# Kernel optimization log

Measured on AMD Instinct MI355X. Metric: run time of the kernel, lower is better.

## Reference

```python
import jax, jax.numpy as jnp
import numpy as np
import math

NO, NR, E = 100000, 1000, 1000000
DO, DR, DE, H, OM = 64, 32, 4, 64, 32


def setup_inputs() -> dict:
    key = jax.random.key(0)
    ks = jax.random.split(key, 20)
    s = lambda k, sh: jax.random.normal(k, sh, dtype=jnp.float32) * 0.05
    inp = {
        'x_order': jax.random.normal(ks[0], (NO, DO), dtype=jnp.float32),
        'x_rider': jax.random.normal(ks[1], (NR, DR), dtype=jnp.float32),
        'edge_attr': jax.random.normal(ks[2], (E, DE), dtype=jnp.float32),
        'order_idx': jax.random.randint(ks[3], (E,), 0, NO),
        'rider_idx': jax.random.randint(ks[4], (E,), 0, NR),
        'omega_encoded': jax.random.normal(ks[5], (OM,), dtype=jnp.float32),
        # TransformerConv params (heads=1)
        'Wk': s(ks[6], (DO, H)), 'bk': jnp.zeros((H,), jnp.float32),
        'Wq': s(ks[7], (DR, H)), 'bq': jnp.zeros((H,), jnp.float32),
        'Wv': s(ks[8], (DO, H)), 'bv': jnp.zeros((H,), jnp.float32),
        'We': s(ks[9], (DE, H)),  # lin_edge, bias=False in PyG
        'Wskip': s(ks[10], (DR, H)), 'bskip': jnp.zeros((H,), jnp.float32),
        # order_proj
        'Wp': s(ks[11], (DO, H)), 'bp': jnp.zeros((H,), jnp.float32),
        # residual MLP: Linear(2H+OM,128) -> ReLU -> Linear(128,1)
        'W1': s(ks[12], (2 * H + OM, 128)), 'b1': jnp.zeros((128,), jnp.float32),
        'W2': s(ks[13], (128, 1)), 'b2': jnp.zeros((1,), jnp.float32),
    }
    return inp


def _segment_softmax(alpha, seg, num_segments):
    m = jax.ops.segment_max(alpha, seg, num_segments=num_segments)
    m = jnp.where(jnp.isfinite(m), m, 0.0)
    ex = jnp.exp(alpha - m[seg])
    denom = jax.ops.segment_sum(ex, seg, num_segments=num_segments)
    return ex / (denom[seg] + 1e-16)


def reference(x_order, x_rider, edge_attr, order_idx, rider_idx, omega_encoded,
              Wk, bk, Wq, bq, Wv, bv, We, Wskip, bskip, Wp, bp, W1, b1, W2, b2):
    scale = 1.0 / math.sqrt(H)
    # TransformerConv((order, rider) -> rider), heads=1, edge_dim
    q = x_rider @ Wq + bq            # [NR, H]
    k = x_order @ Wk + bk            # [NO, H]
    v = x_order @ Wv + bv            # [NO, H]
    e = edge_attr @ We               # [E, H]
    k_j = k[order_idx] + e           # [E, H]
    v_j = v[order_idx] + e           # [E, H]
    alpha = jnp.sum(q[rider_idx] * k_j, axis=-1) * scale  # [E]
    alpha = _segment_softmax(alpha, rider_idx, NR)
    agg = jax.ops.segment_sum(alpha[:, None] * v_j, rider_idx, num_segments=NR)  # [NR, H]
    rider_emb = agg + x_rider @ Wskip + bskip  # root/skip connection

    # edge scoring
    order_proj = x_order @ Wp + bp   # [NO, H]
    oe = order_proj[order_idx]       # [E, H]
    re = rider_emb[rider_idx]        # [E, H]
    dot = jnp.sum(oe * re, axis=-1) * scale  # [E]
    omega_expand = jnp.broadcast_to(omega_encoded[None, :], (oe.shape[0], OM))
    resid_in = jnp.concatenate([oe, re, omega_expand], axis=-1)  # [E, 2H+OM]
    hmid = jax.nn.relu(resid_in @ W1 + b1)
    resid = (hmid @ W2 + b2)[:, 0]
    return jnp.clip(dot + resid, -10.0, 10.0)
```

## Files before the change

kernel.cpp:

```cpp
#include <hip/hip_runtime.h>
#include <hip/hip_bf16.h>
#include <math.h>

#define NO_N 100000
#define NR_N 1000
#define E_N  1000000
#define SB     250
#define SCHUNK 4000
#define KVP_TILES 1563
#define MAXTILES 17008

typedef short bf16x8 __attribute__((ext_vector_type(8)));
typedef float floatx4 __attribute__((ext_vector_type(4)));

__device__ __forceinline__ unsigned short bfu(float x) {
    union { __hip_bfloat16 h; unsigned short u; } c;
    c.h = __float2bfloat16(x);
    return c.u;
}
__device__ __forceinline__ float bflo(unsigned int u) {
    return __uint_as_float(u << 16);
}
__device__ __forceinline__ float bfhi(unsigned int u) {
    return __uint_as_float(u & 0xffff0000u);
}

__global__ __launch_bounds__(256) void k_prep_rider(
    const float* __restrict__ xr,
    const float* __restrict__ Wq, const float* __restrict__ bq,
    const float* __restrict__ Wskip, const float* __restrict__ bskip,
    const float* __restrict__ We,
    float* __restrict__ q, float* __restrict__ skip, float* __restrict__ t)
{
    __shared__ float sx[4][32];
    __shared__ float sq[4][64];
    int tid = threadIdx.x;
    int rbase = blockIdx.x * 4;
    if (tid < 128) {
        int rl = tid >> 5, d = tid & 31;
        int r = rbase + rl;
        sx[rl][d] = (r < NR_N) ? xr[r * 32 + d] : 0.f;
    }
    __syncthreads();
    int rl = tid >> 6, h = tid & 63;
    int r = rbase + rl;
    float aq = bq[h], as = bskip[h];
    #pragma unroll 4
    for (int d = 0; d < 32; ++d) {
        float xv = sx[rl][d];
        aq += xv * Wq[d * 64 + h];
        as += xv * Wskip[d * 64 + h];
    }
    sq[rl][h] = aq;
    if (r < NR_N) { q[r * 64 + h] = aq; skip[r * 64 + h] = as; }
    __syncthreads();
    if (tid < 16) {
        int rl2 = tid >> 2, d = tid & 3;
        int r2 = rbase + rl2;
        float acc = 0.f;
        for (int hh = 0; hh < 64; ++hh) acc += We[d * 64 + hh] * sq[rl2][hh];
        if (r2 < NR_N) t[r2 * 4 + d] = acc;
    }
}

__global__ __launch_bounds__(128) void k_prep_b1eff(
    const float* __restrict__ W1, const float* __restrict__ b1,
    const float* __restrict__ omega, float* __restrict__ b1eff)
{
    int c = threadIdx.x;
    float acc = b1[c];
    #pragma unroll 4
    for (int j = 0; j < 32; ++j) acc += omega[j] * W1[(128 + j) * 128 + c];
    b1eff[c] = acc;
}

__global__ __launch_bounds__(256) void k_kvp(
    const float* __restrict__ x,
    const float* __restrict__ Wk, const float* __restrict__ bk,
    const float* __restrict__ Wv, const float* __restrict__ bv,
    const float* __restrict__ Wp, const float* __restrict__ bp,
    unsigned short* __restrict__ kb, unsigned short* __restrict__ vb,
    unsigned short* __restrict__ pb)
{
    __shared__ __align__(16) unsigned short sX[64 * 72];
    const int tid = threadIdx.x;
    const int wave = tid >> 6, lane = tid & 63;
    const int l15 = lane & 15, quad = lane >> 4;

    bf16x8 bfr[3][2];
    float bias[3];
    unsigned short* outT[3];
    int colc[3];
    #pragma unroll
    for (int ct = 0; ct < 3; ++ct) {
        int n = wave * 48 + ct * 16 + l15;
        int table = n >> 6, c = n & 63;
        const float* W  = (table == 0) ? Wk : (table == 1) ? Wv : Wp;
        const float* bb = (table == 0) ? bk : (table == 1) ? bv : bp;
        bias[ct] = bb[c];
        colc[ct] = c;
        outT[ct] = (table == 0) ? kb : (table == 1) ? vb : pb;
        #pragma unroll
        for (int kf = 0; kf < 2; ++kf) {
            bf16x8 f;
            #pragma unroll
            for (int j = 0; j < 8; ++j)
                f[j] = (short)bfu(W[(size_t)(kf * 32 + quad * 8 + j) * 64 + c]);
            bfr[ct][kf] = f;
        }
    }

    const int srl = tid >> 2;
    const int sqt = (tid & 3) * 16;

    for (int tile = blockIdx.x; tile < KVP_TILES; tile += gridDim.x) {
        int rowbase = tile * 64;
        {
            int row = rowbase + srl;
            unsigned short* dst = sX + srl * 72 + sqt;
            if (row < NO_N) {
                const float4* src = (const float4*)(x + (size_t)row * 64 + sqt);
                #pragma unroll
                for (int i = 0; i < 4; ++i) {
                    float4 a = src[i];
                    ushort4 u = { bfu(a.x), bfu(a.y), bfu(a.z), bfu(a.w) };
                    *(ushort4*)(dst + i * 4) = u;
                }
            } else {
                ushort4 z = {0, 0, 0, 0};
                #pragma unroll
                for (int i = 0; i < 4; ++i) *(ushort4*)(dst + i * 4) = z;
            }
        }
        __syncthreads();

        floatx4 acc[4][3];
        #pragma unroll
        for (int rt = 0; rt < 4; ++rt)
            #pragma unroll
            for (int ct = 0; ct < 3; ++ct)
                acc[rt][ct] = (floatx4){bias[ct], bias[ct], bias[ct], bias[ct]};

        #pragma unroll
        for (int rt = 0; rt < 4; ++rt) {
            const unsigned short* ar = sX + (size_t)(rt * 16 + l15) * 72 + quad * 8;
            bf16x8 a0 = *(const bf16x8*)(ar);
            bf16x8 a1 = *(const bf16x8*)(ar + 32);
            #pragma unroll
            for (int ct = 0; ct < 3; ++ct) {
                floatx4 c = acc[rt][ct];
                c = __builtin_amdgcn_mfma_f32_16x16x32_bf16(a0, bfr[ct][0], c, 0, 0, 0);
                c = __builtin_amdgcn_mfma_f32_16x16x32_bf16(a1, bfr[ct][1], c, 0, 0, 0);
                acc[rt][ct] = c;
            }
        }

        #pragma unroll
        for (int rt = 0; rt < 4; ++rt) {
            int rb = rowbase + rt * 16 + quad * 4;
            #pragma unroll
            for (int ct = 0; ct < 3; ++ct) {
                unsigned short* o = outT[ct];
                size_t cbase = colc[ct];
                #pragma unroll
                for (int g = 0; g < 4; ++g) {
                    int row = rb + g;
                    if (row < NO_N)
                        o[(size_t)row * 64 + cbase] = bfu(acc[rt][ct][g]);
                }
            }
        }
        __syncthreads();
    }
}

__global__ __launch_bounds__(256) void k_hist2(const int* __restrict__ ridx,
                                               int* __restrict__ ghist)
{
    __shared__ int hc[NR_N];
    int tid = threadIdx.x, b = blockIdx.x;
    for (int i = tid; i < NR_N; i += 256) hc[i] = 0;
    __syncthreads();
    int s = b * SCHUNK;
    for (int i = s + tid; i < s + SCHUNK; i += 256)
        atomicAdd(&hc[ridx[i]], 1);
    __syncthreads();
    for (int i = tid; i < NR_N; i += 256)
        ghist[i * SB + b] = hc[i];
}

__global__ __launch_bounds__(256) void k_colscan(const int* __restrict__ ghist,
                                                 int* __restrict__ gpre,
                                                 int* __restrict__ counts)
{
    __shared__ int s[256];
    int tid = threadIdx.x, r = blockIdx.x;
    int v = (tid < SB) ? ghist[r * SB + tid] : 0;
    s[tid] = v;
    __syncthreads();
    for (int off = 1; off < 256; off <<= 1) {
        int tv = (tid >= off) ? s[tid - off] : 0;
        __syncthreads();
        s[tid] += tv;
        __syncthreads();
    }
    if (tid < SB) gpre[r * SB + tid] = s[tid] - v;
    if (tid == 255) counts[r] = s[255];
}

__global__ __launch_bounds__(1024) void k_scan(const int* __restrict__ counts,
                                               int* __restrict__ offsets,
                                               int* __restrict__ tilestart,
                                               int* __restrict__ tile2r)
{
    __shared__ int s[1024];
    int tid = threadIdx.x;
    int c = (tid < NR_N) ? counts[tid] : 0;
    s[tid] = c;
    __syncthreads();
    for (int off = 1; off < 1024; off <<= 1) {
        int tv = (tid >= off) ? s[tid - off] : 0;
        __syncthreads();
        s[tid] += tv;
        __syncthreads();
    }
    if (tid < NR_N) offsets[tid] = s[tid] - c;
    if (tid == NR_N - 1) offsets[NR_N] = s[tid];
    __syncthreads();
    int tc = (tid < NR_N) ? ((c + 63) >> 6) : 0;
    s[tid] = tc;
    __syncthreads();
    for (int off = 1; off < 1024; off <<= 1) {
        int tv = (tid >= off) ? s[tid - off] : 0;
        __syncthreads();
        s[tid] += tv;
        __syncthreads();
    }
    if (tid < NR_N) {
        int ts = s[tid] - tc;
        tilestart[tid] = ts;
        for (int t = 0; t < tc; ++t) tile2r[ts + t] = tid;
    }
    if (tid == NR_N - 1) tilestart[NR_N] = s[tid];
}

__global__ __launch_bounds__(256) void k_scatter2(
    const int* __restrict__ ridx, const int* __restrict__ oidx,
    const float* __restrict__ ea, const float* __restrict__ t,
    const int* __restrict__ offsets, const int* __restrict__ gpre,
    int4* __restrict__ spack, int2* __restrict__ soe)
{
    __shared__ int cur[NR_N];
    int tid = threadIdx.x, b = blockIdx.x;
    for (int i = tid; i < NR_N; i += 256)
        cur[i] = offsets[i] + gpre[i * SB + b];
    __syncthreads();
    int s = b * SCHUNK;
    for (int i = s + tid; i < s + SCHUNK; i += 256) {
        int r = ridx[i];
        int o = oidx[i];
        float4 e4 = *(const float4*)(ea + (size_t)i * 4);
        float4 t4 = *(const float4*)(t + r * 4);
        float h = e4.x * t4.x + e4.y * t4.y + e4.z * t4.z + e4.w * t4.w;
        int pos = atomicAdd(&cur[r], 1);
        int4 pk;
        pk.x = o;
        pk.y = __float_as_int(h);
        pk.z = (int)((unsigned)bfu(e4.x) | ((unsigned)bfu(e4.y) << 16));
        pk.w = (int)((unsigned)bfu(e4.z) | ((unsigned)bfu(e4.w) << 16));
        spack[pos] = pk;
        soe[pos] = make_int2(o, i);
    }
}

__global__ __launch_bounds__(1024) void k_rider(
    const int* __restrict__ offsets, const int4* __restrict__ spack,
    const float* __restrict__ q,
    const unsigned short* __restrict__ kb, const unsigned short* __restrict__ vb,
    const float* __restrict__ We, const float* __restrict__ skip,
    float* __restrict__ emb)
{
    __shared__ float sQ[64];
    __shared__ int2 sOX[16][64];
    __shared__ float rv[16][64];
    __shared__ float re4[16][4];
    __shared__ float rd[16];

    int r = blockIdx.x;
    int wave = threadIdx.x >> 6, lane = threadIdx.x & 63;
    if (threadIdx.x < 64) sQ[threadIdx.x] = q[r * 64 + threadIdx.x];
    __syncthreads();

    int beg = offsets[r], end = offsets[r + 1];
    int cnt = end - beg;
    int chunk = (cnt + 15) >> 4;
    int s0 = beg + wave * chunk;
    int s1 = min(s0 + chunk, end);

    float aggv = 0.f, dsum = 0.f;
    float ag0 = 0.f, ag1 = 0.f, ag2 = 0.f, ag3 = 0.f;
    const float2* sQ2 = (const float2*)sQ;

    for (int jb = s0; jb < s1; jb += 64) {
        int j = jb + lane;
        bool valid = (j < s1);
        int4 pk = make_int4(0, 0, 0, 0);
        if (valid) pk = spack[j];
        int oo = pk.x;
        float h = __int_as_float(pk.y);

        const uint4* krow = (const uint4*)(kb + (size_t)oo * 64);
        uint4 K0 = krow[0], K1 = krow[1], K2 = krow[2], K3 = krow[3];
        uint4 K4 = krow[4], K5 = krow[5], K6 = krow[6], K7 = krow[7];
        float acc = h;
        #define DOT8(Kv, base) { \
            float2 qa = sQ2[(base) + 0]; \
            acc = fmaf(bflo(Kv.x), qa.x, acc); acc = fmaf(bfhi(Kv.x), qa.y, acc); \
            float2 qb = sQ2[(base) + 1]; \
            acc = fmaf(bflo(Kv.y), qb.x, acc); acc = fmaf(bfhi(Kv.y), qb.y, acc); \
            float2 qc = sQ2[(base) + 2]; \
            acc = fmaf(bflo(Kv.z), qc.x, acc); acc = fmaf(bfhi(Kv.z), qc.y, acc); \
            float2 qd = sQ2[(base) + 3]; \
            acc = fmaf(bflo(Kv.w), qd.x, acc); acc = fmaf(bfhi(Kv.w), qd.y, acc); }
        DOT8(K0, 0) DOT8(K1, 4) DOT8(K2, 8) DOT8(K3, 12)
        DOT8(K4, 16) DOT8(K5, 20) DOT8(K6, 24) DOT8(K7, 28)
        #undef DOT8

        float exv = valid ? __expf(acc * 0.125f) : 0.f;
        dsum += exv;
        unsigned int ez = (unsigned int)pk.z, ew = (unsigned int)pk.w;
        ag0 = fmaf(exv, bflo(ez), ag0);
        ag1 = fmaf(exv, bfhi(ez), ag1);
        ag2 = fmaf(exv, bflo(ew), ag2);
        ag3 = fmaf(exv, bfhi(ew), ag3);

        sOX[wave][lane] = make_int2(oo, __float_as_int(exv));

        int nn = min(s1 - jb, 64);
        int i = 0;
        for (; i + 8 <= nn; i += 8) {
            int2 x0 = sOX[wave][i + 0], x1 = sOX[wave][i + 1];
            int2 x2 = sOX[wave][i + 2], x3 = sOX[wave][i + 3];
            int2 x4 = sOX[wave][i + 4], x5 = sOX[wave][i + 5];
            int2 x6 = sOX[wave][i + 6], x7 = sOX[wave][i + 7];
            unsigned short u0 = vb[(size_t)x0.x * 64 + lane];
            unsigned short u1 = vb[(size_t)x1.x * 64 + lane];
            unsigned short u2 = vb[(size_t)x2.x * 64 + lane];
            unsigned short u3 = vb[(size_t)x3.x * 64 + lane];
            unsigned short u4 = vb[(size_t)x4.x * 64 + lane];
            unsigned short u5 = vb[(size_t)x5.x * 64 + lane];
            unsigned short u6 = vb[(size_t)x6.x * 64 + lane];
            unsigned short u7 = vb[(size_t)x7.x * 64 + lane];
            aggv = fmaf(__int_as_float(x0.y), __uint_as_float((unsigned int)u0 << 16), aggv);
            aggv = fmaf(__int_as_float(x1.y), __uint_as_float((unsigned int)u1 << 16), aggv);
            aggv = fmaf(__int_as_float(x2.y), __uint_as_float((unsigned int)u2 << 16), aggv);
            aggv = fmaf(__int_as_float(x3.y), __uint_as_float((unsigned int)u3 << 16), aggv);
            aggv = fmaf(__int_as_float(x4.y), __uint_as_float((unsigned int)u4 << 16), aggv);
            aggv = fmaf(__int_as_float(x5.y), __uint_as_float((unsigned int)u5 << 16), aggv);
            aggv = fmaf(__int_as_float(x6.y), __uint_as_float((unsigned int)u6 << 16), aggv);
            aggv = fmaf(__int_as_float(x7.y), __uint_as_float((unsigned int)u7 << 16), aggv);
        }
        for (; i < nn; ++i) {
            int2 xx = sOX[wave][i];
            unsigned short uu = vb[(size_t)xx.x * 64 + lane];
            aggv = fmaf(__int_as_float(xx.y), __uint_as_float((unsigned int)uu << 16), aggv);
        }
    }

    #pragma unroll
    for (int m = 1; m < 64; m <<= 1) {
        dsum += __shfl_xor(dsum, m);
        ag0 += __shfl_xor(ag0, m);
        ag1 += __shfl_xor(ag1, m);
        ag2 += __shfl_xor(ag2, m);
        ag3 += __shfl_xor(ag3, m);
    }

    rv[wave][lane] = aggv;
    if (lane == 0) {
        rd[wave] = dsum;
        re4[wave][0] = ag0; re4[wave][1] = ag1;
        re4[wave][2] = ag2; re4[wave][3] = ag3;
    }
    __syncthreads();
    if (threadIdx.x < 64) {
        int l = threadIdx.x;
        float av = 0.f, ds = 0.f, a0 = 0.f, a1 = 0.f, a2 = 0.f, a3 = 0.f;
        #pragma unroll 4
        for (int w = 0; w < 16; ++w) {
            av += rv[w][l]; ds += rd[w];
            a0 += re4[w][0]; a1 += re4[w][1]; a2 += re4[w][2]; a3 += re4[w][3];
        }
        float corr = a0 * We[0 * 64 + l] + a1 * We[1 * 64 + l]
                   + a2 * We[2 * 64 + l] + a3 * We[3 * 64 + l];
        emb[r * 64 + l] = (av + corr) / (ds + 1e-16f) + skip[r * 64 + l];
    }
}

__global__ __launch_bounds__(256) void k_br(
    const float* __restrict__ emb, const float* __restrict__ W1,
    const float* __restrict__ b1eff, float* __restrict__ Br)
{
    int wave = threadIdx.x >> 6, lane = threadIdx.x & 63;
    int r = blockIdx.x * 4 + wave;
    if (r >= NR_N) return;
    float a0 = b1eff[lane], a1 = b1eff[64 + lane];
    #pragma unroll 8
    for (int d = 0; d < 64; ++d) {
        float ev = emb[r * 64 + d];
        a0 = fmaf(ev, W1[(size_t)(64 + d) * 128 + lane], a0);
        a1 = fmaf(ev, W1[(size_t)(64 + d) * 128 + 64 + lane], a1);
    }
    Br[r * 128 + lane] = a0;
    Br[r * 128 + 64 + lane] = a1;
}

__global__ __launch_bounds__(256) void k_edge2(
    const int2* __restrict__ soe, const int* __restrict__ offsets,
    const int* __restrict__ tilestart, const int* __restrict__ tile2r,
    const unsigned short* __restrict__ pb, const float* __restrict__ emb,
    const float* __restrict__ Br, const float* __restrict__ W1,
    const float* __restrict__ W2, const float* __restrict__ b2,
    float* __restrict__ out)
{
    __shared__ __align__(16) unsigned short sA[64 * 72];
    __shared__ float sDot[64];
    __shared__ int   sE[64];
    __shared__ float sPart[4][64];

    const int tid = threadIdx.x;
    const int wave = tid >> 6;
    const int lane = tid & 63;
    const int l15 = lane & 15;
    const int quad = lane >> 4;

    bf16x8 bfr[2][2];
    float w2v[2];
    #pragma unroll
    for (int ctl = 0; ctl < 2; ++ctl) {
        int n = wave * 32 + ctl * 16 + l15;
        w2v[ctl] = W2[n];
        #pragma unroll
        for (int kc = 0; kc < 2; ++kc) {
            bf16x8 f;
            #pragma unroll
            for (int j = 0; j < 8; ++j)
                f[j] = (short)bfu(W1[(size_t)(kc * 32 + quad * 8 + j) * 128 + n]);
            bfr[ctl][kc] = f;
        }
    }
    float b2v = b2[0];
    const int ntiles = tilestart[NR_N];

    const int el = tid >> 2;
    const int q16 = (tid & 3) * 16;

    for (int tile = blockIdx.x; tile < ntiles; tile += gridDim.x) {
        int r = tile2r[tile];
        int jb = offsets[r] + ((tile - tilestart[r]) << 6);
        int jend = offsets[r + 1];

        {
            int j = jb + el;
            int o = 0, e = -1;
            if (j < jend) { int2 oe = soe[j]; o = oe.x; e = oe.y; }
            const uint4* po = (const uint4*)(pb + (size_t)o * 64 + q16);
            uint4 A0 = po[0], A1 = po[1];
            const float4* pe = (const float4*)(emb + r * 64 + q16);
            float4 e0 = pe[0], e1 = pe[1], e2 = pe[2], e3 = pe[3];
            float dotp;
            dotp  = bflo(A0.x) * e0.x + bfhi(A0.x) * e0.y;
            dotp += bflo(A0.y) * e0.z + bfhi(A0.y) * e0.w;
            dotp += bflo(A0.z) * e1.x + bfhi(A0.z) * e1.y;
            dotp += bflo(A0.w) * e1.z + bfhi(A0.w) * e1.w;
            dotp += bflo(A1.x) * e2.x + bfhi(A1.x) * e2.y;
            dotp += bflo(A1.y) * e2.z + bfhi(A1.y) * e2.w;
            dotp += bflo(A1.z) * e3.x + bfhi(A1.z) * e3.y;
            dotp += bflo(A1.w) * e3.z + bfhi(A1.w) * e3.w;
            uint4* sp = (uint4*)(sA + el * 72 + q16);
            sp[0] = A0; sp[1] = A1;
            dotp += __shfl_xor(dotp, 1);
            dotp += __shfl_xor(dotp, 2);
            if ((tid & 3) == 0) { sDot[el] = dotp; sE[el] = e; }
        }
        __syncthreads();

        float brv[2];
        #pragma unroll
        for (int ctl = 0; ctl < 2; ++ctl)
            brv[ctl] = Br[r * 128 + wave * 32 + ctl * 16 + l15];

        floatx4 acc[4][2];
        #pragma unroll
        for (int rt = 0; rt < 4; ++rt)
            #pragma unroll
            for (int ctl = 0; ctl < 2; ++ctl)
                acc[rt][ctl] = (floatx4){0.f, 0.f, 0.f, 0.f};

        #pragma unroll
        for (int rt = 0; rt < 4; ++rt) {
            const unsigned short* ar = sA + (size_t)(rt * 16 + l15) * 72 + quad * 8;
            bf16x8 a0 = *(const bf16x8*)(ar);
            bf16x8 a1 = *(const bf16x8*)(ar + 32);
            #pragma unroll
            for (int ctl = 0; ctl < 2; ++ctl) {
                floatx4 c = acc[rt][ctl];
                c = __builtin_amdgcn_mfma_f32_16x16x32_bf16(a0, bfr[ctl][0], c, 0, 0, 0);
                c = __builtin_amdgcn_mfma_f32_16x16x32_bf16(a1, bfr[ctl][1], c, 0, 0, 0);
                acc[rt][ctl] = c;
            }
        }

        #pragma unroll
        for (int rt = 0; rt < 4; ++rt) {
            floatx4 s;
            #pragma unroll
            for (int g = 0; g < 4; ++g)
                s[g] = fmaxf(acc[rt][0][g] + brv[0], 0.f) * w2v[0]
                     + fmaxf(acc[rt][1][g] + brv[1], 0.f) * w2v[1];
            #pragma unroll
            for (int m = 1; m < 16; m <<= 1) {
                s[0] += __shfl_xor(s[0], m);
                s[1] += __shfl_xor(s[1], m);
                s[2] += __shfl_xor(s[2], m);
                s[3] += __shfl_xor(s[3], m);
            }
            if (l15 == 0) {
                int rowb = rt * 16 + quad * 4;
                sPart[wave][rowb + 0] = s[0];
                sPart[wave][rowb + 1] = s[1];
                sPart[wave][rowb + 2] = s[2];
                sPart[wave][rowb + 3] = s[3];
            }
        }
        __syncthreads();
        if (tid < 64) {
            int e = sE[tid];
            if (e >= 0) {
                float v = sPart[0][tid] + sPart[1][tid] + sPart[2][tid] + sPart[3][tid]
                        + 0.125f * sDot[tid] + b2v;
                out[e] = fminf(fmaxf(v, -10.f), 10.f);
            }
        }
        __syncthreads();
    }
}

extern "C" void kernel_launch(void* const* d_in, const int* in_sizes, int n_in,
                              void* d_out, int out_size, void* d_ws, size_t ws_size,
                              hipStream_t stream)
{
    const float* x_order   = (const float*)d_in[0];
    const float* x_rider   = (const float*)d_in[1];
    const float* edge_attr = (const float*)d_in[2];
    const int*   order_idx = (const int*)d_in[3];
    const int*   rider_idx = (const int*)d_in[4];
    const float* omega     = (const float*)d_in[5];
    const float* Wk = (const float*)d_in[6];  const float* bk = (const float*)d_in[7];
    const float* Wq = (const float*)d_in[8];  const float* bq = (const float*)d_in[9];
    const float* Wv = (const float*)d_in[10]; const float* bv = (const float*)d_in[11];
    const float* We = (const float*)d_in[12];
    const float* Wskip = (const float*)d_in[13]; const float* bskip = (const float*)d_in[14];
    const float* Wp = (const float*)d_in[15]; const float* bp = (const float*)d_in[16];
    const float* W1 = (const float*)d_in[17]; const float* b1 = (const float*)d_in[18];
    const float* W2 = (const float*)d_in[19]; const float* b2 = (const float*)d_in[20];
    float* out = (float*)d_out;

    unsigned short* ws_kb = (unsigned short*)d_ws;
    unsigned short* ws_vb = ws_kb + (size_t)NO_N * 64;
    unsigned short* ws_pb = ws_vb + (size_t)NO_N * 64;
    int4* ws_spack = (int4*)(ws_pb + (size_t)NO_N * 64);
    int2* ws_soe   = (int2*)(ws_spack + E_N);
    float* wsf     = (float*)(ws_soe + E_N);
    float* ws_q    = wsf;
    float* ws_skip = ws_q + NR_N * 64;
    float* ws_emb  = ws_skip + NR_N * 64;
    float* ws_t    = ws_emb + NR_N * 64;
    float* ws_b1e  = ws_t + NR_N * 4;
    float* ws_Br   = ws_b1e + 128;
    int* ws_counts  = (int*)(ws_Br + NR_N * 128);
    int* ws_offsets = ws_counts + NR_N;
    int* ws_tilest  = ws_offsets + NR_N + 8;
    int* ws_tile2r  = ws_tilest + NR_N + 8;
    int* ws_ghist   = ws_tile2r + MAXTILES;
    int* ws_gpre    = ws_ghist + NR_N * SB;

    k_prep_rider<<<NR_N / 4, 256, 0, stream>>>(x_rider, Wq, bq, Wskip, bskip, We,
                                               ws_q, ws_skip, ws_t);
    k_prep_b1eff<<<1, 128, 0, stream>>>(W1, b1, omega, ws_b1e);
    k_kvp<<<521, 256, 0, stream>>>(x_order, Wk, bk, Wv, bv, Wp, bp,
                                   ws_kb, ws_vb, ws_pb);
    k_hist2<<<SB, 256, 0, stream>>>(rider_idx, ws_ghist);
    k_colscan<<<NR_N, 256, 0, stream>>>(ws_ghist, ws_gpre, ws_counts);
    k_scan<<<1, 1024, 0, stream>>>(ws_counts, ws_offsets, ws_tilest, ws_tile2r);
    k_scatter2<<<SB, 256, 0, stream>>>(rider_idx, order_idx, edge_attr, ws_t,
                                       ws_offsets, ws_gpre, ws_spack, ws_soe);
    k_rider<<<NR_N, 1024, 0, stream>>>(ws_offsets, ws_spack, ws_q,
                                       ws_kb, ws_vb, We, ws_skip, ws_emb);
    k_br<<<NR_N / 4, 256, 0, stream>>>(ws_emb, W1, ws_b1e, ws_Br);
    k_edge2<<<2048, 256, 0, stream>>>(ws_soe, ws_offsets, ws_tilest, ws_tile2r,
                                      ws_pb, ws_emb, ws_Br, W1, W2, b2, out);
}
```

Before: 325.5 us.

## Merge front kernels, fuse Br into rider kernel, restructure edge MLP with permuted writes

Merges the rider prep, b1eff, KVP projection and histogram kernels into one launch by dispatching on block index, and folds the Br computation into the rider aggregation kernel, which removes several launches. The edge kernel now has each wave process 16 rows across all 128 hidden columns. This drops the cross-wave partial-sum shared memory and two block barriers. It writes results in sorted order to a temp buffer, and a new permutation kernel gathers them back into edge order. The trade-off is more registers per wave in the edge kernel plus an extra pass over E elements for the permutation.

Measured after the change: 312.6 us. 4.0% less time.

```diff
diff --git a/kernel.cpp b/kernel.cpp
--- a/kernel.cpp
+++ b/kernel.cpp
@@ -8,6 +8,7 @@
 #define SB     250
 #define SCHUNK 4000
 #define KVP_TILES 1563
+#define KVP_BLKS 521
 #define MAXTILES 17008
 
 typedef short bf16x8 __attribute__((ext_vector_type(8)));
@@ -25,168 +26,165 @@
     return __uint_as_float(u & 0xffff0000u);
 }
 
-__global__ __launch_bounds__(256) void k_prep_rider(
+__global__ __launch_bounds__(256) void k_front(
     const float* __restrict__ xr,
     const float* __restrict__ Wq, const float* __restrict__ bq,
     const float* __restrict__ Wskip, const float* __restrict__ bskip,
     const float* __restrict__ We,
-    float* __restrict__ q, float* __restrict__ skip, float* __restrict__ t)
-{
-    __shared__ float sx[4][32];
-    __shared__ float sq[4][64];
-    int tid = threadIdx.x;
-    int rbase = blockIdx.x * 4;
-    if (tid < 128) {
-        int rl = tid >> 5, d = tid & 31;
-        int r = rbase + rl;
-        sx[rl][d] = (r < NR_N) ? xr[r * 32 + d] : 0.f;
-    }
-    __syncthreads();
-    int rl = tid >> 6, h = tid & 63;
-    int r = rbase + rl;
-    float aq = bq[h], as = bskip[h];
-    #pragma unroll 4
-    for (int d = 0; d < 32; ++d) {
-        float xv = sx[rl][d];
-        aq += xv * Wq[d * 64 + h];
-        as += xv * Wskip[d * 64 + h];
-    }
-    sq[rl][h] = aq;
-    if (r < NR_N) { q[r * 64 + h] = aq; skip[r * 64 + h] = as; }
-    __syncthreads();
-    if (tid < 16) {
-        int rl2 = tid >> 2, d = tid & 3;
-        int r2 = rbase + rl2;
-        float acc = 0.f;
-        for (int hh = 0; hh < 64; ++hh) acc += We[d * 64 + hh] * sq[rl2][hh];
-        if (r2 < NR_N) t[r2 * 4 + d] = acc;
-    }
-}
-
-__global__ __launch_bounds__(128) void k_prep_b1eff(
+    float* __restrict__ q, float* __restrict__ skip, float* __restrict__ t,
     const float* __restrict__ W1, const float* __restrict__ b1,
-    const float* __restrict__ omega, float* __restrict__ b1eff)
-{
-    int c = threadIdx.x;
-    float acc = b1[c];
-    #pragma unroll 4
-    for (int j = 0; j < 32; ++j) acc += omega[j] * W1[(128 + j) * 128 + c];
-    b1eff[c] = acc;
-}
-
-__global__ __launch_bounds__(256) void k_kvp(
+    const float* __restrict__ omega, float* __restrict__ b1eff,
     const float* __restrict__ x,
     const float* __restrict__ Wk, const float* __restrict__ bk,
     const float* __restrict__ Wv, const float* __restrict__ bv,
     const float* __restrict__ Wp, const float* __restrict__ bp,
     unsigned short* __restrict__ kb, unsigned short* __restrict__ vb,
-    unsigned short* __restrict__ pb)
-{
-    __shared__ __align__(16) unsigned short sX[64 * 72];
+    unsigned short* __restrict__ pb,
+    const int* __restrict__ ridx, int* __restrict__ ghist)
+{
+    __shared__ __align__(16) char smem[9216];
     const int tid = threadIdx.x;
-    const int wave = tid >> 6, lane = tid & 63;
-    const int l15 = lane & 15, quad = lane >> 4;
-
-    bf16x8 bfr[3][2];
-    float bias[3];
-    unsigned short* outT[3];
-    int colc[3];
-    #pragma unroll
-    for (int ct = 0; ct < 3; ++ct) {
-        int n = wave * 48 + ct * 16 + l15;
-        int table = n >> 6, c = n & 63;
-        const float* W  = (table == 0) ? Wk : (table == 1) ? Wv : Wp;
-        const float* bb = (table == 0) ? bk : (table == 1) ? bv : bp;
-        bias[ct] = bb[c];
-        colc[ct] = c;
-        outT[ct] = (table == 0) ? kb : (table == 1) ? vb : pb;
+    const int b = blockIdx.x;
+
+    if (b < 250) {
+        float* sx = (float*)smem;
+        float* sq = sx + 128;
+        int rbase = b * 4;
+        if (tid < 128) {
+            int rl = tid >> 5, d = tid & 31;
+            sx[rl * 32 + d] = xr[(rbase + rl) * 32 + d];
+        }
+        __syncthreads();
+        int rl = tid >> 6, h = tid & 63;
+        int r = rbase + rl;
+        float aq = bq[h], as = bskip[h];
+        #pragma unroll 4
+        for (int d = 0; d < 32; ++d) {
+            float xv = sx[rl * 32 + d];
+            aq += xv * Wq[d * 64 + h];
+            as += xv * Wskip[d * 64 + h];
+        }
+        sq[rl * 64 + h] = aq;
+        q[r * 64 + h] = aq;
+        skip[r * 64 + h] = as;
+        __syncthreads();
+        if (tid < 16) {
+            int rl2 = tid >> 2, d = tid & 3;
+            float acc = 0.f;
+            for (int hh = 0; hh < 64; ++hh)
+                acc += We[d * 64 + hh] * sq[rl2 * 64 + hh];
+            t[(rbase + rl2) * 4 + d] = acc;
+        }
+    } else if (b == 250) {
+        if (tid < 128) {
+            float acc = b1[tid];
+            #pragma unroll 4
+            for (int j = 0; j < 32; ++j)
+                acc += omega[j] * W1[(128 + j) * 128 + tid];
+            b1eff[tid] = acc;
+        }
+    } else if (b < 251 + KVP_BLKS) {
+        unsigned short* sX = (unsigned short*)smem;
+        const int wave = tid >> 6, lane = tid & 63;
+        const int l15 = lane & 15, quad = lane >> 4;
+
+        bf16x8 bfr[3][2];
+        float bias[3];
+        unsigned short* outT[3];
+        int colc[3];
         #pragma unroll
-        for (int kf = 0; kf < 2; ++kf) {
-            bf16x8 f;
-            #pragma unroll
-            for (int j = 0; j < 8; ++j)
-                f[j] = (short)bfu(W[(size_t)(kf * 32 + quad * 8 + j) * 64 + c]);
-            bfr[ct][kf] = f;
-        }
-    }
-
-    const int srl = tid >> 2;
-    const int sqt = (tid & 3) * 16;
-
-    for (int tile = blockIdx.x; tile < KVP_TILES; tile += gridDim.x) {
-        int rowbase = tile * 64;
-        {
-            int row = rowbase + srl;
-            unsigned short* dst = sX + srl * 72 + sqt;
-            if (row < NO_N) {
-                const float4* src = (const float4*)(x + (size_t)row * 64 + sqt);
+        for (int ct = 0; ct < 3; ++ct) {
+            int n = wave * 48 + ct * 16 + l15;
+            int table = n >> 6, c = n & 63;
+            const float* W  = (table == 0) ? Wk : (table == 1) ? Wv : Wp;
+            const float* bb = (table == 0) ? bk : (table == 1) ? bv : bp;
+            bias[ct] = bb[c];
+            colc[ct] = c;
+            outT[ct] = (table == 0) ? kb : (table == 1) ? vb : pb;
+            #pragma unroll
+            for (int kf = 0; kf < 2; ++kf) {
+                bf16x8 f;
                 #pragma unroll
-                for (int i = 0; i < 4; ++i) {
-                    float4 a = src[i];
-                    ushort4 u = { bfu(a.x), bfu(a.y), bfu(a.z), bfu(a.w) };
-                    *(ushort4*)(dst + i * 4) = u;
-                }
-            } else {
-                ushort4 z = {0, 0, 0, 0};
-                #pragma unroll
-                for (int i = 0; i < 4; ++i) *(ushort4*)(dst + i * 4) = z;
+                for (int j = 0; j < 8; ++j)
+                    f[j] = (short)bfu(W[(size_t)(kf * 32 + quad * 8 + j) * 64 + c]);
+                bfr[ct][kf] = f;
             }
         }
-        __syncthreads();
-
-        floatx4 acc[4][3];
-        #pragma unroll
-        for (int rt = 0; rt < 4; ++rt)
-            #pragma unroll
-            for (int ct = 0; ct < 3; ++ct)
-                acc[rt][ct] = (floatx4){bias[ct], bias[ct], bias[ct], bias[ct]};
-
-        #pragma unroll
-        for (int rt = 0; rt < 4; ++rt) {
-            const unsigned short* ar = sX + (size_t)(rt * 16 + l15) * 72 + quad * 8;
-            bf16x8 a0 = *(const bf16x8*)(ar);
-            bf16x8 a1 = *(const bf16x8*)(ar + 32);
-            #pragma unroll
-            for (int ct = 0; ct < 3; ++ct) {
-                floatx4 c = acc[rt][ct];
-                c = __builtin_amdgcn_mfma_f32_16x16x32_bf16(a0, bfr[ct][0], c, 0, 0, 0);
-                c = __builtin_amdgcn_mfma_f32_16x16x32_bf16(a1, bfr[ct][1], c, 0, 0, 0);
-                acc[rt][ct] = c;
-            }
-        }
-
-        #pragma unroll
-        for (int rt = 0; rt < 4; ++rt) {
-            int rb = rowbase + rt * 16 + quad * 4;
-            #pragma unroll
-            for (int ct = 0; ct < 3; ++ct) {
-                unsigned short* o = outT[ct];
-                size_t cbase = colc[ct];
-                #pragma unroll
-                for (int g = 0; g < 4; ++g) {
-                    int row = rb + g;
-                    if (row < NO_N)
-                        o[(size_t)row * 64 + cbase] = bfu(acc[rt][ct][g]);
+
+        const int srl = tid >> 2;
+        const int sqt = (tid & 3) * 16;
+
+        for (int tile = b - 251; tile < KVP_TILES; tile += KVP_BLKS) {
+            int rowbase = tile * 64;
+            {
+                int row = rowbase + srl;
+                unsigned short* dst = sX + srl * 72 + sqt;
+                if (row < NO_N) {
+                    const float4* src = (const float4*)(x + (size_t)row * 64 + sqt);
+                    #pragma unroll
+                    for (int i = 0; i < 4; ++i) {
+                        float4 a = src[i];
+                        ushort4 u = { bfu(a.x), bfu(a.y), bfu(a.z), bfu(a.w) };
+                        *(ushort4*)(dst + i * 4) = u;
+                    }
+                } else {
+                    ushort4 z = {0, 0, 0, 0};
+                    #pragma unroll
+                    for (int i = 0; i < 4; ++i) *(ushort4*)(dst + i * 4) = z;
                 }
             }
-        }
-        __syncthreads();
-    }
-}
-
-__global__ __launch_bounds__(256) void k_hist2(const int* __restrict__ ridx,
-                                               int* __restrict__ ghist)
-{
-    __shared__ int hc[NR_N];
-    int tid = threadIdx.x, b = blockIdx.x;
-    for (int i = tid; i < NR_N; i += 256) hc[i] = 0;
-    __syncthreads();
-    int s = b * SCHUNK;
-    for (int i = s + tid; i < s + SCHUNK; i += 256)
-        atomicAdd(&hc[ridx[i]], 1);
-    __syncthreads();
-    for (int i = tid; i < NR_N; i += 256)
-        ghist[i * SB + b] = hc[i];
+            __syncthreads();
+
+            floatx4 acc[4][3];
+            #pragma unroll
+            for (int rt = 0; rt < 4; ++rt)
+                #pragma unroll
+                for (int ct = 0; ct < 3; ++ct)
+                    acc[rt][ct] = (floatx4){bias[ct], bias[ct], bias[ct], bias[ct]};
+
+            #pragma unroll
+            for (int rt = 0; rt < 4; ++rt) {
+                const unsigned short* ar = sX + (size_t)(rt * 16 + l15) * 72 + quad * 8;
+                bf16x8 a0 = *(const bf16x8*)(ar);
+                bf16x8 a1 = *(const bf16x8*)(ar + 32);
+                #pragma unroll
+                for (int ct = 0; ct < 3; ++ct) {
+                    floatx4 c = acc[rt][ct];
+                    c = __builtin_amdgcn_mfma_f32_16x16x32_bf16(a0, bfr[ct][0], c, 0, 0, 0);
+                    c = __builtin_amdgcn_mfma_f32_16x16x32_bf16(a1, bfr[ct][1], c, 0, 0, 0);
+                    acc[rt][ct] = c;
+                }
+            }
+
+            #pragma unroll
+            for (int rt = 0; rt < 4; ++rt) {
+                int rb = rowbase + rt * 16 + quad * 4;
+                #pragma unroll
+                for (int ct = 0; ct < 3; ++ct) {
+                    unsigned short* o = outT[ct];
+                    size_t cbase = colc[ct];
+                    #pragma unroll
+                    for (int g = 0; g < 4; ++g) {
+                        int row = rb + g;
+                        if (row < NO_N)
+                            o[(size_t)row * 64 + cbase] = bfu(acc[rt][ct][g]);
+                    }
+                }
+            }
+            __syncthreads();
+        }
+    } else {
+        int* hc = (int*)smem;
+        int hb = b - (251 + KVP_BLKS);
+        for (int i = tid; i < NR_N; i += 256) hc[i] = 0;
+        __syncthreads();
+        int s = hb * SCHUNK;
+        for (int i = s + tid; i < s + SCHUNK; i += 256)
+            atomicAdd(&hc[ridx[i]], 1);
+        __syncthreads();
+        for (int i = tid; i < NR_N; i += 256)
+            ghist[i * SB + hb] = hc[i];
+    }
 }
 
 __global__ __launch_bounds__(256) void k_colscan(const int* __restrict__ ghist,
@@ -248,7 +246,7 @@
     const int* __restrict__ ridx, const int* __restrict__ oidx,
     const float* __restrict__ ea, const float* __restrict__ t,
     const int* __restrict__ offsets, const int* __restrict__ gpre,
-    int4* __restrict__ spack, int2* __restrict__ soe)
+    int4* __restrict__ spack, int* __restrict__ so, int* __restrict__ rank)
 {
     __shared__ int cur[NR_N];
     int tid = threadIdx.x, b = blockIdx.x;
@@ -269,7 +267,8 @@
         pk.z = (int)((unsigned)bfu(e4.x) | ((unsigned)bfu(e4.y) << 16));
         pk.w = (int)((unsigned)bfu(e4.z) | ((unsigned)bfu(e4.w) << 16));
         spack[pos] = pk;
-        soe[pos] = make_int2(o, i);
+        so[pos] = o;
+        rank[i] = pos;
     }
 }
 
@@ -278,7 +277,8 @@
     const float* __restrict__ q,
     const unsigned short* __restrict__ kb, const unsigned short* __restrict__ vb,
     const float* __restrict__ We, const float* __restrict__ skip,
-    float* __restrict__ emb)
+    const float* __restrict__ W1, const float* __restrict__ b1eff,
+    float* __restrict__ emb, float* __restrict__ Br)
 {
     __shared__ float sQ[64];
     __shared__ int2 sOX[16][64];
@@ -393,40 +393,31 @@
         }
         float corr = a0 * We[0 * 64 + l] + a1 * We[1 * 64 + l]
                    + a2 * We[2 * 64 + l] + a3 * We[3 * 64 + l];
-        emb[r * 64 + l] = (av + corr) / (ds + 1e-16f) + skip[r * 64 + l];
-    }
-}
-
-__global__ __launch_bounds__(256) void k_br(
-    const float* __restrict__ emb, const float* __restrict__ W1,
-    const float* __restrict__ b1eff, float* __restrict__ Br)
-{
-    int wave = threadIdx.x >> 6, lane = threadIdx.x & 63;
-    int r = blockIdx.x * 4 + wave;
-    if (r >= NR_N) return;
-    float a0 = b1eff[lane], a1 = b1eff[64 + lane];
-    #pragma unroll 8
-    for (int d = 0; d < 64; ++d) {
-        float ev = emb[r * 64 + d];
-        a0 = fmaf(ev, W1[(size_t)(64 + d) * 128 + lane], a0);
-        a1 = fmaf(ev, W1[(size_t)(64 + d) * 128 + 64 + lane], a1);
-    }
-    Br[r * 128 + lane] = a0;
-    Br[r * 128 + 64 + lane] = a1;
-}
-
-__global__ __launch_bounds__(256) void k_edge2(
-    const int2* __restrict__ soe, const int* __restrict__ offsets,
+        float val = (av + corr) / (ds + 1e-16f) + skip[r * 64 + l];
+        emb[r * 64 + l] = val;
+        sQ[l] = val;
+    }
+    __syncthreads();
+    if (threadIdx.x < 128) {
+        int c = threadIdx.x;
+        float a = b1eff[c];
+        #pragma unroll 8
+        for (int d = 0; d < 64; ++d)
+            a = fmaf(sQ[d], W1[(size_t)(64 + d) * 128 + c], a);
+        Br[r * 128 + c] = a;
+    }
+}
+
+__global__ __launch_bounds__(256, 3) void k_edge2(
+    const int* __restrict__ so, const int* __restrict__ offsets,
     const int* __restrict__ tilestart, const int* __restrict__ tile2r,
     const unsigned short* __restrict__ pb, const float* __restrict__ emb,
     const float* __restrict__ Br, const float* __restrict__ W1,
     const float* __restrict__ W2, const float* __restrict__ b2,
-    float* __restrict__ out)
+    float* __restrict__ tmp)
 {
     __shared__ __align__(16) unsigned short sA[64 * 72];
     __shared__ float sDot[64];
-    __shared__ int   sE[64];
-    __shared__ float sPart[4][64];
 
     const int tid = threadIdx.x;
     const int wave = tid >> 6;
@@ -434,11 +425,11 @@
     const int l15 = lane & 15;
     const int quad = lane >> 4;
 
-    bf16x8 bfr[2][2];
-    float w2v[2];
+    bf16x8 bfr[8][2];
+    float w2v[8];
     #pragma unroll
-    for (int ctl = 0; ctl < 2; ++ctl) {
-        int n = wave * 32 + ctl * 16 + l15;
+    for (int ctl = 0; ctl < 8; ++ctl) {
+        int n = ctl * 16 + l15;
         w2v[ctl] = W2[n];
         #pragma unroll
         for (int kc = 0; kc < 2; ++kc) {
@@ -462,8 +453,7 @@
 
         {
             int j = jb + el;
-            int o = 0, e = -1;
-            if (j < jend) { int2 oe = soe[j]; o = oe.x; e = oe.y; }
+            int o = so[min(j, jend - 1)];
             const uint4* po = (const uint4*)(pb + (size_t)o * 64 + q16);
             uint4 A0 = po[0], A1 = po[1];
             const float4* pe = (const float4*)(emb + r * 64 + q16);
@@ -481,69 +471,62 @@
             sp[0] = A0; sp[1] = A1;
             dotp += __shfl_xor(dotp, 1);
             dotp += __shfl_xor(dotp, 2);
-            if ((tid & 3) == 0) { sDot[el] = dotp; sE[el] = e; }
-        }
-        __syncthreads();
-
-        float brv[2];
+            if ((tid & 3) == 0) sDot[el] = dotp;
+        }
+
+        const unsigned short* ar = sA + (size_t)(wave * 16 + l15) * 72 + quad * 8;
+        bf16x8 a0 = *(const bf16x8*)(ar);
+        bf16x8 a1 = *(const bf16x8*)(ar + 32);
+        floatx4 acc[8];
         #pragma unroll
-        for (int ctl = 0; ctl < 2; ++ctl)
-            brv[ctl] = Br[r * 128 + wave * 32 + ctl * 16 + l15];
-
-        floatx4 acc[4][2];
+        for (int ctl = 0; ctl < 8; ++ctl) {
+            floatx4 c = (floatx4){0.f, 0.f, 0.f, 0.f};
+            c = __builtin_amdgcn_mfma_f32_16x16x32_bf16(a0, bfr[ctl][0], c, 0, 0, 0);
+            c = __builtin_amdgcn_mfma_f32_16x16x32_bf16(a1, bfr[ctl][1], c, 0, 0, 0);
+            acc[ctl] = c;
+        }
+
+        float brv[8];
         #pragma unroll
-        for (int rt = 0; rt < 4; ++rt)
-            #pragma unroll
-            for (int ctl = 0; ctl < 2; ++ctl)
-                acc[rt][ctl] = (floatx4){0.f, 0.f, 0.f, 0.f};
-
+        for (int ctl = 0; ctl < 8; ++ctl)
+            brv[ctl] = Br[r * 128 + ctl * 16 + l15];
+
+        floatx4 s;
         #pragma unroll
-        for (int rt = 0; rt < 4; ++rt) {
-            const unsigned short* ar = sA + (size_t)(rt * 16 + l15) * 72 + quad * 8;
-            bf16x8 a0 = *(const bf16x8*)(ar);
-            bf16x8 a1 = *(const bf16x8*)(ar + 32);
-            #pragma unroll
-            for (int ctl = 0; ctl < 2; ++ctl) {
-                floatx4 c = acc[rt][ctl];
-                c = __builtin_amdgcn_mfma_f32_16x16x32_bf16(a0, bfr[ctl][0], c, 0, 0, 0);
-                c = __builtin_amdgcn_mfma_f32_16x16x32_bf16(a1, bfr[ctl][1], c, 0, 0, 0);
-                acc[rt][ctl] = c;
+        for (int g = 0; g < 4; ++g) {
+            float v = 0.f;
+            #pragma unroll
+            for (int ctl = 0; ctl < 8; ++ctl)
+                v = fmaf(fmaxf(acc[ctl][g] + brv[ctl], 0.f), w2v[ctl], v);
+            s[g] = v;
+        }
+        #pragma unroll
+        for (int m = 1; m < 16; m <<= 1) {
+            s[0] += __shfl_xor(s[0], m);
+            s[1] += __shfl_xor(s[1], m);
+            s[2] += __shfl_xor(s[2], m);
+            s[3] += __shfl_xor(s[3], m);
+        }
+        if (l15 == 0) {
+            int rowb = wave * 16 + quad * 4;
+            #pragma unroll
+            for (int g = 0; g < 4; ++g) {
+                int pos = jb + rowb + g;
+                if (pos < jend) {
+                    float v = s[g] + 0.125f * sDot[rowb + g] + b2v;
+                    tmp[pos] = fminf(fmaxf(v, -10.f), 10.f);
+                }
             }
         }
-
-        #pragma unroll
-        for (int rt = 0; rt < 4; ++rt) {
-            floatx4 s;
-            #pragma unroll
-            for (int g = 0; g < 4; ++g)
-                s[g] = fmaxf(acc[rt][0][g] + brv[0], 0.f) * w2v[0]
-                     + fmaxf(acc[rt][1][g] + brv[1], 0.f) * w2v[1];
-            #pragma unroll
-            for (int m = 1; m < 16; m <<= 1) {
-                s[0] += __shfl_xor(s[0], m);
-                s[1] += __shfl_xor(s[1], m);
-                s[2] += __shfl_xor(s[2], m);
-                s[3] += __shfl_xor(s[3], m);
-            }
-            if (l15 == 0) {
-                int rowb = rt * 16 + quad * 4;
-                sPart[wave][rowb + 0] = s[0];
-                sPart[wave][rowb + 1] = s[1];
-                sPart[wave][rowb + 2] = s[2];
-                sPart[wave][rowb + 3] = s[3];
-            }
-        }
-        __syncthreads();
-        if (tid < 64) {
-            int e = sE[tid];
-            if (e >= 0) {
-                float v = sPart[0][tid] + sPart[1][tid] + sPart[2][tid] + sPart[3][tid]
-                        + 0.125f * sDot[tid] + b2v;
-                out[e] = fminf(fmaxf(v, -10.f), 10.f);
-            }
-        }
-        __syncthreads();
-    }
+    }
+}
+
+__global__ __launch_bounds__(256) void k_perm(const int* __restrict__ rank,
+                                              const float* __restrict__ tmp,
+                                              float* __restrict__ out)
+{
+    int i = blockIdx.x * 256 + threadIdx.x;
+    if (i < E_N) out[i] = tmp[rank[i]];
 }
 
 extern "C" void kernel_launch(void* const* d_in, const int* in_sizes, int n_in,
@@ -570,8 +553,10 @@
     unsigned short* ws_vb = ws_kb + (size_t)NO_N * 64;
     unsigned short* ws_pb = ws_vb + (size_t)NO_N * 64;
     int4* ws_spack = (int4*)(ws_pb + (size_t)NO_N * 64);
-    int2* ws_soe   = (int2*)(ws_spack + E_N);
-    float* wsf     = (float*)(ws_soe + E_N);
+    float* ws_tmp  = (float*)ws_spack;
+    int*  ws_so    = (int*)(ws_spack + E_N);
+    int*  ws_rank  = ws_so + E_N;
+    float* wsf     = (float*)(ws_rank + E_N);
     float* ws_q    = wsf;
     float* ws_skip = ws_q + NR_N * 64;
     float* ws_emb  = ws_skip + NR_N * 64;
@@ -585,19 +570,19 @@
     int* ws_ghist   = ws_tile2r + MAXTILES;
     int* ws_gpre    = ws_ghist + NR_N * SB;
 
-    k_prep_rider<<<NR_N / 4, 256, 0, stream>>>(x_rider, Wq, bq, Wskip, bskip, We,
-                                               ws_q, ws_skip, ws_t);
-    k_prep_b1eff<<<1, 128, 0, stream>>>(W1, b1, omega, ws_b1e);
-    k_kvp<<<521, 256, 0, stream>>>(x_order, Wk, bk, Wv, bv, Wp, bp,
-                                   ws_kb, ws_vb, ws_pb);
-    k_hist2<<<SB, 256, 0, stream>>>(rider_idx, ws_ghist);
+    k_front<<<251 + KVP_BLKS + SB, 256, 0, stream>>>(
+        x_rider, Wq, bq, Wskip, bskip, We, ws_q, ws_skip, ws_t,
+        W1, b1, omega, ws_b1e,
+        x_order, Wk, bk, Wv, bv, Wp, bp, ws_kb, ws_vb, ws_pb,
+        rider_idx, ws_ghist);
     k_colscan<<<NR_N, 256, 0, stream>>>(ws_ghist, ws_gpre, ws_counts);
     k_scan<<<1, 1024, 0, stream>>>(ws_counts, ws_offsets, ws_tilest, ws_tile2r);
     k_scatter2<<<SB, 256, 0, stream>>>(rider_idx, order_idx, edge_attr, ws_t,
-                                       ws_offsets, ws_gpre, ws_spack, ws_soe);
+                                       ws_offsets, ws_gpre, ws_spack, ws_so, ws_rank);
     k_rider<<<NR_N, 1024, 0, stream>>>(ws_offsets, ws_spack, ws_q,
-                                       ws_kb, ws_vb, We, ws_skip, ws_emb);
-    k_br<<<NR_N / 4, 256, 0, stream>>>(ws_emb, W1, ws_b1e, ws_Br);
-    k_edge2<<<2048, 256, 0, stream>>>(ws_soe, ws_offsets, ws_tilest, ws_tile2r,
-                                      ws_pb, ws_emb, ws_Br, W1, W2, b2, out);
-}
+                                       ws_kb, ws_vb, We, ws_skip,
+                                       W1, ws_b1e, ws_emb, ws_Br);
+    k_edge2<<<2048, 256, 0, stream>>>(ws_so, ws_offsets, ws_tilest, ws_tile2r,
+                                      ws_pb, ws_emb, ws_Br, W1, W2, b2, ws_tmp);
+    k_perm<<<(E_N + 255) / 256, 256, 0, stream>>>(ws_rank, ws_tmp, out);
+}
```
